# Performance work log

Measured on AMD Instinct MI355X. Metric: run time of the kernel, lower is better.

The kernel has to match this reference:

```python
import jax, jax.numpy as jnp
import numpy as np

QUANT_RANGE = 2688.0  # 6 (max E2M1) * 448 (max E4M3), tllm static_6 rule
EPS = 1e-12
BLOCK = 16  # NVFP4 block size along K


def _round_e2m1(v):
    # Round to the E2M1 grid {0, .5, 1, 1.5, 2, 3, 4, 6} (signed), RTNE on the grid.
    a = jnp.abs(v)
    # quantization step doubles with the exponent: 0.5 for |a|<2, 1 for [2,4), 2 for [4,6]
    e = jnp.floor(jnp.log2(jnp.maximum(a, 1e-30)))
    step = jnp.exp2(jnp.maximum(e, 0.0) - 1.0)
    q = jnp.minimum(jnp.round(a / step) * step, 6.0)
    return jnp.sign(v) * q


def _round_e4m3(v):
    # FP8 E4M3 round-trip (block scale factors are stored as E4M3)
    return v.astype(jnp.float8_e4m3fn).astype(jnp.float32)


def _fp4_quantize(t2d, global_scale):
    # t2d: [R, K] -> (e2m1 codes [R, K/16, 16], e4m3 block scales [R, K/16])
    R, K = t2d.shape
    tb = t2d.reshape(R, K // BLOCK, BLOCK)
    block_amax = jnp.max(jnp.abs(tb), axis=-1)            # [R, K/16]
    sf = _round_e4m3(block_amax * global_scale / 6.0)      # FP8 scale per block
    sf_safe = jnp.maximum(sf, EPS)
    q = _round_e2m1(tb * (global_scale / sf_safe)[..., None])
    return q, sf


def _nvfp4_linear(x, weight, bias):
    in_features = weight.shape[1]
    out_features = weight.shape[0]
    orig_shape = x.shape
    x2 = x.reshape(-1, in_features)                        # [M, K]
    M = x2.shape[0]

    # weight quantization (done once at from_linear time in the original)
    w_amax = jnp.maximum(jnp.max(jnp.abs(weight)), EPS)
    w_gs = QUANT_RANGE / w_amax
    qw, sfw = _fp4_quantize(weight, w_gs)                  # [N, K/16, 16], [N, K/16]

    # dynamic activation quantization
    a_amax = jnp.maximum(jnp.max(jnp.abs(x2)), EPS)
    a_gs = QUANT_RANGE / a_amax
    qx, sfx = _fp4_quantize(x2, a_gs)                      # [M, K/16, 16], [M, K/16]

    # alpha = act_amax * (weight_amax / quant_range^2)
    alpha = a_amax * w_amax / (QUANT_RANGE * QUANT_RANGE)

    # block-scaled GEMM: out[m,n] = alpha * sum_b sfx[m,b] sfw[n,b] (qx[m,b,:] . qw[n,b,:])
    # fused as a dense GEMM over per-block-scaled codes (mathematically identical)
    dx = (qx * sfx[..., None]).reshape(M, in_features)
    dw = (qw * sfw[..., None]).reshape(out_features, in_features)
    out = alpha * (dx @ dw.T) + bias
    return out.reshape(*orig_shape[:-1], out_features)


def setup_inputs() -> dict:
    key = jax.random.key(0)
    k1, k2, k3 = jax.random.split(key, 3)
    x = jax.random.normal(k1, (2, 2048, 4096), dtype=jnp.float32)
    weight = jax.random.normal(k2, (4096, 4096), dtype=jnp.float32) * 0.02
    bias = jax.random.normal(k3, (4096,), dtype=jnp.float32) * 0.01
    return {"x": x, "weight": weight, "bias": bias}


def reference(x, weight, bias):
    return _nvfp4_linear(x, weight, bias)
```

## Files before the change

### kernel.cpp

```cpp
#include <hip/hip_runtime.h>
#include <hip/hip_bf16.h>


typedef unsigned short u16;
typedef __bf16 bf16x8 __attribute__((ext_vector_type(8)));
typedef float f32x4 __attribute__((ext_vector_type(4)));
typedef unsigned short u16x8 __attribute__((ext_vector_type(8)));

#define GLD_LDS(gsrc, ldst)                                                     \
  __builtin_amdgcn_global_load_lds(                                             \
      (const __attribute__((address_space(1))) void*)(gsrc),                    \
      (__attribute__((address_space(3))) void*)(ldst), 16, 0, 0)

#define SBAR()                                                                  \
  do {                                                                          \
    asm volatile("" ::: "memory");                                              \
    __builtin_amdgcn_s_barrier();                                               \
    asm volatile("" ::: "memory");                                              \
  } while (0)

#define KEEP4(S) asm volatile("" ::"v"(S[0]), "v"(S[1]), "v"(S[2]), "v"(S[3]))


__device__ __forceinline__ float round_e4m3(float v) {
  if (v < 0.015625f) {
    return rintf(v * 512.0f) * 0.001953125f;
  }
  unsigned b = __float_as_uint(v);
  unsigned e = (b >> 23) & 0xFFu;
  float step = __uint_as_float((e - 3u) << 23);
  return rintf(v / step) * step;
}

__device__ __forceinline__ float round_e2m1(float v) {
  float a = fabsf(v);
  float step = (a < 2.0f) ? 0.5f : ((a < 4.0f) ? 1.0f : 2.0f);
  float q = fminf(rintf(a / step) * step, 6.0f);
  return copysignf(q, v);
}


__global__ void nvfp4_amax_kernel(const float* __restrict__ x,
                                  const float* __restrict__ w,
                                  unsigned* __restrict__ sc, int nx4, int nw4) {
  const float4* src = blockIdx.y ? (const float4*)w : (const float4*)x;
  int n4 = blockIdx.y ? nw4 : nx4;
  float m = 0.f;
  for (int i = blockIdx.x * blockDim.x + threadIdx.x; i < n4;
       i += gridDim.x * blockDim.x) {
    float4 v = src[i];
    m = fmaxf(m, fmaxf(fmaxf(fabsf(v.x), fabsf(v.y)),
                       fmaxf(fabsf(v.z), fabsf(v.w))));
  }
#pragma unroll
  for (int off = 32; off; off >>= 1) m = fmaxf(m, __shfl_down(m, off));
  __shared__ float red[4];
  if ((threadIdx.x & 63) == 0) red[threadIdx.x >> 6] = m;
  __syncthreads();
  if (threadIdx.x == 0) {
    m = fmaxf(fmaxf(red[0], red[1]), fmaxf(red[2], red[3]));
    atomicMax(&sc[blockIdx.y], __float_as_uint(m));
  }
}


__global__ void nvfp4_quant_kernel(const float* __restrict__ x,
                                   const float* __restrict__ w,
                                   u16* __restrict__ dx, u16* __restrict__ dw,
                                   const unsigned* __restrict__ sc,
                                   int nx4, int nw4) {
  int g = blockIdx.x * blockDim.x + threadIdx.x;
  const float* src; u16* dst; int which, i4;
  if (g < nx4) { src = x; dst = dx; which = 0; i4 = g; }
  else {
    i4 = g - nx4; if (i4 >= nw4) return;
    src = w; dst = dw; which = 1;
  }
  float4 v = ((const float4*)src)[i4];

  float m = fmaxf(fmaxf(fabsf(v.x), fabsf(v.y)), fmaxf(fabsf(v.z), fabsf(v.w)));
  m = fmaxf(m, __shfl_xor(m, 1));
  m = fmaxf(m, __shfl_xor(m, 2));

  float amax = fmaxf(__uint_as_float(sc[which]), 1e-12f);
  float gs = 2688.0f / amax;
  float sf = round_e4m3((m * gs) / 6.0f);
  float sfs = fmaxf(sf, 1e-12f);
  float r = gs / sfs;

  ushort4 o;
  o.x = (u16)(__float_as_uint(round_e2m1(v.x * r) * sf) >> 16);
  o.y = (u16)(__float_as_uint(round_e2m1(v.y * r) * sf) >> 16);
  o.z = (u16)(__float_as_uint(round_e2m1(v.z * r) * sf) >> 16);
  o.w = (u16)(__float_as_uint(round_e2m1(v.w * r) * sf) >> 16);
  ((ushort4*)dst)[i4] = o;
}


#define BM 256
#define BN 256
#define BK 32

__global__ __launch_bounds__(512, 2) void nvfp4_gemm_kernel(
    const u16* __restrict__ A,
    const u16* __restrict__ B,
    const float* __restrict__ bias, const unsigned* __restrict__ sc,
    float* __restrict__ C, int M, int N, int K) {
  __shared__ u16 lA[4][BM * BK];
  __shared__ u16 lB[4][BN * BK];

  const int tid = threadIdx.x;
  const int lane = tid & 63;
  const int wv = tid >> 6;
  const int wm = wv >> 2;
  const int wn = wv & 3;

  const int bid = blockIdx.x;
  const int xcd = bid & 7, loc = bid >> 3;
  const int tm0 = ((xcd & 3) * 4 + (loc & 3)) * BM;
  const int tn0 = ((xcd >> 2) * 8 + (loc >> 2)) * BN;

  const int srow = tid >> 2;
  const int skey = (srow >> 1) & 3;
  const int scol = ((tid & 3) ^ skey) * 8;
  const u16* gA0 = A + (size_t)(tm0 + srow) * K + scol;
  const u16* gA1 = A + (size_t)(tm0 + 128 + srow) * K + scol;
  const u16* gB0 = B + (size_t)(tn0 + srow) * K + scol;
  const u16* gB1 = B + (size_t)(tn0 + 128 + srow) * K + scol;
  const int ld0 = tid * 8;
  const int ld1 = tid * 8 + 4096;

#define STAGE_A(tt)                                                             \
  do {                                                                          \
    int _b = (tt) & 3;                                                          \
    GLD_LDS(gA0 + (size_t)(tt) * BK, &lA[_b][ld0]);                             \
    GLD_LDS(gA1 + (size_t)(tt) * BK, &lA[_b][ld1]);                             \
  } while (0)
#define STAGE_B(tt)                                                             \
  do {                                                                          \
    int _b = (tt) & 3;                                                          \
    GLD_LDS(gB0 + (size_t)(tt) * BK, &lB[_b][ld0]);                             \
    GLD_LDS(gB1 + (size_t)(tt) * BK, &lB[_b][ld1]);                             \
  } while (0)

  const int rb = lane & 15;
  const int cc = (((lane >> 4) ^ ((rb >> 1) & 3)) << 3);
  const int arow = wm * 128 + rb;
  const int brow = wn * 64 + rb;

  f32x4 acc[8][4] = {};
  const int NT = K / BK;
  const int NG = NT / 2;

  STAGE_A(0); STAGE_B(0);
  STAGE_A(1); STAGE_B(1);
  STAGE_A(2); STAGE_B(2);
  asm volatile("s_waitcnt vmcnt(8)" ::: "memory");
  SBAR();

  bf16x8 av[4], aw[4], bve[4], bvo[4];

  for (int g = 0; g < NG; ++g) {
    const int t0 = 2 * g, t1 = 2 * g + 1;
    const int s0 = 2 * g + 3, s1 = 2 * g + 4;
    const u16* bufA0 = lA[t0 & 3];
    const u16* bufB0 = lB[t0 & 3];
    const u16* bufA1 = lA[t1 & 3];
    const u16* bufB1 = lB[t1 & 3];

#pragma unroll
    for (int j = 0; j < 4; ++j)
      bve[j] = *(const bf16x8*)(bufB0 + (brow + j * 16) * BK + cc);
#pragma unroll
    for (int i = 0; i < 4; ++i)
      av[i] = *(const bf16x8*)(bufA0 + (arow + i * 16) * BK + cc);
    if (s0 < NT) STAGE_A(s0);
    SBAR();
    __builtin_amdgcn_s_setprio(1);
#pragma unroll
    for (int i = 0; i < 4; ++i)
#pragma unroll
      for (int j = 0; j < 4; ++j)
        acc[i][j] = __builtin_amdgcn_mfma_f32_16x16x32_bf16(av[i], bve[j],
                                                            acc[i][j], 0, 0, 0);
    __builtin_amdgcn_s_setprio(0);
    SBAR();

#pragma unroll
    for (int i = 0; i < 4; ++i)
      aw[i] = *(const bf16x8*)(bufA0 + (arow + 64 + i * 16) * BK + cc);
    if (s0 < NT) STAGE_B(s0);
    SBAR();
    __builtin_amdgcn_s_setprio(1);
#pragma unroll
    for (int i = 0; i < 4; ++i)
#pragma unroll
      for (int j = 0; j < 4; ++j)
        acc[4 + i][j] = __builtin_amdgcn_mfma_f32_16x16x32_bf16(aw[i], bve[j],
                                                                acc[4 + i][j],
                                                                0, 0, 0);
    __builtin_amdgcn_s_setprio(0);
    KEEP4(av);
    if (g < NG - 1) asm volatile("s_waitcnt vmcnt(8)" ::: "memory");
    else            asm volatile("s_waitcnt vmcnt(0)" ::: "memory");
    SBAR();

#pragma unroll
    for (int j = 0; j < 4; ++j)
      bvo[j] = *(const bf16x8*)(bufB1 + (brow + j * 16) * BK + cc);
#pragma unroll
    for (int i = 0; i < 4; ++i)
      av[i] = *(const bf16x8*)(bufA1 + (arow + i * 16) * BK + cc);
    if (s1 < NT) STAGE_A(s1);
    SBAR();
    __builtin_amdgcn_s_setprio(1);
#pragma unroll
    for (int i = 0; i < 4; ++i)
#pragma unroll
      for (int j = 0; j < 4; ++j)
        acc[i][j] = __builtin_amdgcn_mfma_f32_16x16x32_bf16(av[i], bvo[j],
                                                            acc[i][j], 0, 0, 0);
    __builtin_amdgcn_s_setprio(0);
    SBAR();

#pragma unroll
    for (int i = 0; i < 4; ++i)
      aw[i] = *(const bf16x8*)(bufA1 + (arow + 64 + i * 16) * BK + cc);
    if (s1 < NT) STAGE_B(s1);
    SBAR();
    __builtin_amdgcn_s_setprio(1);
#pragma unroll
    for (int i = 0; i < 4; ++i)
#pragma unroll
      for (int j = 0; j < 4; ++j)
        acc[4 + i][j] = __builtin_amdgcn_mfma_f32_16x16x32_bf16(aw[i], bvo[j],
                                                                acc[4 + i][j],
                                                                0, 0, 0);
    __builtin_amdgcn_s_setprio(0);
    KEEP4(bve);
    KEEP4(av);
    KEEP4(aw);
    if (g < NG - 2)       asm volatile("s_waitcnt vmcnt(8)" ::: "memory");
    else if (g == NG - 2) asm volatile("s_waitcnt vmcnt(4)" ::: "memory");
    SBAR();
  }

  float ax = fmaxf(__uint_as_float(sc[0]), 1e-12f);
  float aw_ = fmaxf(__uint_as_float(sc[1]), 1e-12f);
  float alpha = (ax * aw_) / 7225344.0f;

  const int orow = (lane >> 4) * 4;
  const int ocol = lane & 15;
#pragma unroll
  for (int ai = 0; ai < 8; ++ai) {
#pragma unroll
    for (int j = 0; j < 4; ++j) {
      int col = tn0 + wn * 64 + j * 16 + ocol;
      float bvv = bias[col];
#pragma unroll
      for (int rr = 0; rr < 4; ++rr) {
        int row = tm0 + wm * 128 + ai * 16 + orow + rr;
        C[(size_t)row * N + col] = alpha * acc[ai][j][rr] + bvv;
      }
    }
  }
#undef STAGE_A
#undef STAGE_B
}


extern "C" void kernel_launch(void* const* d_in, const int* in_sizes, int n_in,
                              void* d_out, int out_size, void* d_ws, size_t ws_size,
                              hipStream_t stream) {
  const float* x = (const float*)d_in[0];
  const float* w = (const float*)d_in[1];
  const float* bias = (const float*)d_in[2];
  float* out = (float*)d_out;

  const int N = in_sizes[2];
  const int K = in_sizes[1] / N;
  const int M = in_sizes[0] / K;

  unsigned char* ws = (unsigned char*)d_ws;
  unsigned* sc = (unsigned*)ws;
  u16* dx = (u16*)(ws + 256);
  u16* dw = (u16*)(ws + 256 + (size_t)M * K * sizeof(u16));

  hipMemsetAsync(sc, 0, 8, stream);

  const int nx4 = M * K / 4, nw4 = N * K / 4;
  nvfp4_amax_kernel<<<dim3(1024, 2), 256, 0, stream>>>(x, w, sc, nx4, nw4);

  nvfp4_quant_kernel<<<(nx4 + nw4 + 255) / 256, 256, 0, stream>>>(
      x, w, dx, dw, sc, nx4, nw4);

  nvfp4_gemm_kernel<<<dim3((M / BM) * (N / BN)), 512, 0, stream>>>(
      dx, dw, bias, sc, out, M, N, K);
}
```

Before: 197.0 us.

## Shrink GEMM tile to 256x128 with 4 waves and triple-buffered LDS

The bf16 GEMM moves from a 256x256 tile with 8 waves and a 4-stage LDS ring to a 256x128 tile with 4 waves and a 3-stage ring. Block-to-tile mapping, staging addresses and waitcnt counts are rebuilt to match. The aim is to double the block count for better CU fill and to cut LDS per block so more blocks fit per CU. The cost is less operand reuse per block, more global traffic for A, and a shallower prefetch pipeline.

```diff
diff --git a/kernel.cpp b/kernel.cpp
--- a/kernel.cpp
+++ b/kernel.cpp
@@ -5,7 +5,6 @@
 typedef unsigned short u16;
 typedef __bf16 bf16x8 __attribute__((ext_vector_type(8)));
 typedef float f32x4 __attribute__((ext_vector_type(4)));
-typedef unsigned short u16x8 __attribute__((ext_vector_type(8)));
 
 #define GLD_LDS(gsrc, ldst)                                                     \
   __builtin_amdgcn_global_load_lds(                                             \
@@ -18,8 +17,6 @@
     __builtin_amdgcn_s_barrier();                                               \
     asm volatile("" ::: "memory");                                              \
   } while (0)
-
-#define KEEP4(S) asm volatile("" ::"v"(S[0]), "v"(S[1]), "v"(S[2]), "v"(S[3]))
 
 
 __device__ __forceinline__ float round_e4m3(float v) {
@@ -98,151 +95,149 @@
 
 
 #define BM 256
-#define BN 256
+#define BN 128
 #define BK 32
 
-__global__ __launch_bounds__(512, 2) void nvfp4_gemm_kernel(
+__global__ __launch_bounds__(256, 2) void nvfp4_gemm_kernel(
     const u16* __restrict__ A,
     const u16* __restrict__ B,
     const float* __restrict__ bias, const unsigned* __restrict__ sc,
     float* __restrict__ C, int M, int N, int K) {
-  __shared__ u16 lA[4][BM * BK];
-  __shared__ u16 lB[4][BN * BK];
+  __shared__ u16 lA[3][BM * BK];
+  __shared__ u16 lB[3][BN * BK];
 
   const int tid = threadIdx.x;
   const int lane = tid & 63;
   const int wv = tid >> 6;
-  const int wm = wv >> 2;
-  const int wn = wv & 3;
+  const int wm = wv >> 1;
+  const int wn = wv & 1;
 
   const int bid = blockIdx.x;
   const int xcd = bid & 7, loc = bid >> 3;
-  const int tm0 = ((xcd & 3) * 4 + (loc & 3)) * BM;
-  const int tn0 = ((xcd >> 2) * 8 + (loc >> 2)) * BN;
-
-  const int srow = tid >> 2;
-  const int skey = (srow >> 1) & 3;
-  const int scol = ((tid & 3) ^ skey) * 8;
-  const u16* gA0 = A + (size_t)(tm0 + srow) * K + scol;
-  const u16* gA1 = A + (size_t)(tm0 + 128 + srow) * K + scol;
-  const u16* gB0 = B + (size_t)(tn0 + srow) * K + scol;
-  const u16* gB1 = B + (size_t)(tn0 + 128 + srow) * K + scol;
-  const int ld0 = tid * 8;
-  const int ld1 = tid * 8 + 4096;
-
-#define STAGE_A(tt)                                                             \
+  const int tm0 = (xcd * 2 + (loc >> 5)) * BM;
+  const int tn0 = (loc & 31) * BN;
+
+  const int r4 = lane >> 2;
+  const int swz = ((lane & 3) ^ ((lane >> 3) & 3)) * 8;
+  const u16* gAa[4]; const u16* gBb[2];
+#pragma unroll
+  for (int i = 0; i < 4; ++i)
+    gAa[i] = A + (size_t)(tm0 + (i * 4 + wv) * 16 + r4) * K + swz;
+#pragma unroll
+  for (int i = 0; i < 2; ++i)
+    gBb[i] = B + (size_t)(tn0 + (i * 4 + wv) * 16 + r4) * K + swz;
+  const int ldw = wv * 512 + lane * 8;
+
+#define STAGE_A(tt, bf)                                                         \
   do {                                                                          \
-    int _b = (tt) & 3;                                                          \
-    GLD_LDS(gA0 + (size_t)(tt) * BK, &lA[_b][ld0]);                             \
-    GLD_LDS(gA1 + (size_t)(tt) * BK, &lA[_b][ld1]);                             \
+    _Pragma("unroll") for (int _i = 0; _i < 4; ++_i)                            \
+        GLD_LDS(gAa[_i] + (size_t)(tt) * BK, &lA[bf][_i * 2048 + ldw]);         \
   } while (0)
-#define STAGE_B(tt)                                                             \
+#define STAGE_B(tt, bf)                                                         \
   do {                                                                          \
-    int _b = (tt) & 3;                                                          \
-    GLD_LDS(gB0 + (size_t)(tt) * BK, &lB[_b][ld0]);                             \
-    GLD_LDS(gB1 + (size_t)(tt) * BK, &lB[_b][ld1]);                             \
+    _Pragma("unroll") for (int _i = 0; _i < 2; ++_i)                            \
+        GLD_LDS(gBb[_i] + (size_t)(tt) * BK, &lB[bf][_i * 2048 + ldw]);         \
   } while (0)
 
   const int rb = lane & 15;
   const int cc = (((lane >> 4) ^ ((rb >> 1) & 3)) << 3);
-  const int arow = wm * 128 + rb;
-  const int brow = wn * 64 + rb;
+  const int aoff = (wm * 128 + rb) * BK + cc;
+  const int boff = (wn * 64 + rb) * BK + cc;
 
   f32x4 acc[8][4] = {};
   const int NT = K / BK;
   const int NG = NT / 2;
 
-  STAGE_A(0); STAGE_B(0);
-  STAGE_A(1); STAGE_B(1);
-  STAGE_A(2); STAGE_B(2);
-  asm volatile("s_waitcnt vmcnt(8)" ::: "memory");
+  STAGE_A(0, 0); STAGE_B(0, 0);
+  STAGE_A(1, 1); STAGE_B(1, 1);
+  asm volatile("s_waitcnt vmcnt(6)" ::: "memory");
   SBAR();
 
-  bf16x8 av[4], aw[4], bve[4], bvo[4];
+  bf16x8 av[4], aw[4], bv[4];
+  int cur = 0;
 
   for (int g = 0; g < NG; ++g) {
-    const int t0 = 2 * g, t1 = 2 * g + 1;
-    const int s0 = 2 * g + 3, s1 = 2 * g + 4;
-    const u16* bufA0 = lA[t0 & 3];
-    const u16* bufB0 = lB[t0 & 3];
-    const u16* bufA1 = lA[t1 & 3];
-    const u16* bufB1 = lB[t1 & 3];
+    int t1b = cur + 1; if (t1b == 3) t1b = 0;
+    int s0b = t1b + 1; if (s0b == 3) s0b = 0;
+    const int s0 = 2 * g + 2, s1 = 2 * g + 3;
+    const u16* bufA0 = lA[cur];
+    const u16* bufB0 = lB[cur];
+    const u16* bufA1 = lA[t1b];
+    const u16* bufB1 = lB[t1b];
+    const bool st = (g < NG - 1);
 
 #pragma unroll
     for (int j = 0; j < 4; ++j)
-      bve[j] = *(const bf16x8*)(bufB0 + (brow + j * 16) * BK + cc);
-#pragma unroll
-    for (int i = 0; i < 4; ++i)
-      av[i] = *(const bf16x8*)(bufA0 + (arow + i * 16) * BK + cc);
-    if (s0 < NT) STAGE_A(s0);
-    SBAR();
-    __builtin_amdgcn_s_setprio(1);
-#pragma unroll
-    for (int i = 0; i < 4; ++i)
-#pragma unroll
-      for (int j = 0; j < 4; ++j)
-        acc[i][j] = __builtin_amdgcn_mfma_f32_16x16x32_bf16(av[i], bve[j],
+      bv[j] = *(const bf16x8*)(bufB0 + boff + j * 512);
+#pragma unroll
+    for (int i = 0; i < 4; ++i)
+      av[i] = *(const bf16x8*)(bufA0 + aoff + i * 512);
+    if (st) STAGE_A(s0, s0b);
+    SBAR();
+    __builtin_amdgcn_s_setprio(1);
+#pragma unroll
+    for (int i = 0; i < 4; ++i)
+#pragma unroll
+      for (int j = 0; j < 4; ++j)
+        acc[i][j] = __builtin_amdgcn_mfma_f32_16x16x32_bf16(av[i], bv[j],
                                                             acc[i][j], 0, 0, 0);
     __builtin_amdgcn_s_setprio(0);
     SBAR();
 
 #pragma unroll
     for (int i = 0; i < 4; ++i)
-      aw[i] = *(const bf16x8*)(bufA0 + (arow + 64 + i * 16) * BK + cc);
-    if (s0 < NT) STAGE_B(s0);
-    SBAR();
-    __builtin_amdgcn_s_setprio(1);
-#pragma unroll
-    for (int i = 0; i < 4; ++i)
-#pragma unroll
-      for (int j = 0; j < 4; ++j)
-        acc[4 + i][j] = __builtin_amdgcn_mfma_f32_16x16x32_bf16(aw[i], bve[j],
+      aw[i] = *(const bf16x8*)(bufA0 + aoff + 2048 + i * 512);
+    if (st) STAGE_B(s0, s0b);
+    SBAR();
+    __builtin_amdgcn_s_setprio(1);
+#pragma unroll
+    for (int i = 0; i < 4; ++i)
+#pragma unroll
+      for (int j = 0; j < 4; ++j)
+        acc[4 + i][j] = __builtin_amdgcn_mfma_f32_16x16x32_bf16(aw[i], bv[j],
                                                                 acc[4 + i][j],
                                                                 0, 0, 0);
     __builtin_amdgcn_s_setprio(0);
-    KEEP4(av);
-    if (g < NG - 1) asm volatile("s_waitcnt vmcnt(8)" ::: "memory");
-    else            asm volatile("s_waitcnt vmcnt(0)" ::: "memory");
+    if (st) asm volatile("s_waitcnt vmcnt(6)" ::: "memory");
+    else    asm volatile("s_waitcnt vmcnt(0)" ::: "memory");
     SBAR();
 
 #pragma unroll
     for (int j = 0; j < 4; ++j)
-      bvo[j] = *(const bf16x8*)(bufB1 + (brow + j * 16) * BK + cc);
-#pragma unroll
-    for (int i = 0; i < 4; ++i)
-      av[i] = *(const bf16x8*)(bufA1 + (arow + i * 16) * BK + cc);
-    if (s1 < NT) STAGE_A(s1);
-    SBAR();
-    __builtin_amdgcn_s_setprio(1);
-#pragma unroll
-    for (int i = 0; i < 4; ++i)
-#pragma unroll
-      for (int j = 0; j < 4; ++j)
-        acc[i][j] = __builtin_amdgcn_mfma_f32_16x16x32_bf16(av[i], bvo[j],
+      bv[j] = *(const bf16x8*)(bufB1 + boff + j * 512);
+#pragma unroll
+    for (int i = 0; i < 4; ++i)
+      av[i] = *(const bf16x8*)(bufA1 + aoff + i * 512);
+    if (st) STAGE_A(s1, cur);
+    SBAR();
+    __builtin_amdgcn_s_setprio(1);
+#pragma unroll
+    for (int i = 0; i < 4; ++i)
+#pragma unroll
+      for (int j = 0; j < 4; ++j)
+        acc[i][j] = __builtin_amdgcn_mfma_f32_16x16x32_bf16(av[i], bv[j],
                                                             acc[i][j], 0, 0, 0);
     __builtin_amdgcn_s_setprio(0);
     SBAR();
 
 #pragma unroll
     for (int i = 0; i < 4; ++i)
-      aw[i] = *(const bf16x8*)(bufA1 + (arow + 64 + i * 16) * BK + cc);
-    if (s1 < NT) STAGE_B(s1);
-    SBAR();
-    __builtin_amdgcn_s_setprio(1);
-#pragma unroll
-    for (int i = 0; i < 4; ++i)
-#pragma unroll
-      for (int j = 0; j < 4; ++j)
-        acc[4 + i][j] = __builtin_amdgcn_mfma_f32_16x16x32_bf16(aw[i], bvo[j],
+      aw[i] = *(const bf16x8*)(bufA1 + aoff + 2048 + i * 512);
+    if (st) STAGE_B(s1, cur);
+    SBAR();
+    __builtin_amdgcn_s_setprio(1);
+#pragma unroll
+    for (int i = 0; i < 4; ++i)
+#pragma unroll
+      for (int j = 0; j < 4; ++j)
+        acc[4 + i][j] = __builtin_amdgcn_mfma_f32_16x16x32_bf16(aw[i], bv[j],
                                                                 acc[4 + i][j],
                                                                 0, 0, 0);
     __builtin_amdgcn_s_setprio(0);
-    KEEP4(bve);
-    KEEP4(av);
-    KEEP4(aw);
-    if (g < NG - 2)       asm volatile("s_waitcnt vmcnt(8)" ::: "memory");
-    else if (g == NG - 2) asm volatile("s_waitcnt vmcnt(4)" ::: "memory");
-    SBAR();
+    if (st) asm volatile("s_waitcnt vmcnt(6)" ::: "memory");
+    SBAR();
+
+    cur = s0b;
   }
 
   float ax = fmaxf(__uint_as_float(sc[0]), 1e-12f);
@@ -294,6 +289,6 @@
   nvfp4_quant_kernel<<<(nx4 + nw4 + 255) / 256, 256, 0, stream>>>(
       x, w, dx, dw, sc, nx4, nw4);
 
-  nvfp4_gemm_kernel<<<dim3((M / BM) * (N / BN)), 512, 0, stream>>>(
+  nvfp4_gemm_kernel<<<dim3((M / BM) * (N / BN)), 256, 0, stream>>>(
       dx, dw, bias, sc, out, M, N, K);
 }
```

Measured after the change: 207.1 us. +5.2%, slower.

## Switch GEMM inner loop from 16x16x32 to 32x32x16 bf16 MFMA tiles

Applied to the files above, without the earlier changes.

Replaces the 16x16x32 MFMA tiling with 32x32x16 MFMA instructions. The LDS fragment reads, the LDS XOR swizzle key and the accumulator/epilogue row mapping all change to match. Larger MFMA tiles give more math per fragment read and fewer LDS reads per FLOP. In exchange the epilogue scatters 16 rows per lane with a different store pattern, and the correctness of the new swizzle depends on matching the LDS write and read keys.

```diff
diff --git a/kernel.cpp b/kernel.cpp
--- a/kernel.cpp
+++ b/kernel.cpp
@@ -4,8 +4,7 @@
 
 typedef unsigned short u16;
 typedef __bf16 bf16x8 __attribute__((ext_vector_type(8)));
-typedef float f32x4 __attribute__((ext_vector_type(4)));
-typedef unsigned short u16x8 __attribute__((ext_vector_type(8)));
+typedef float f32x16 __attribute__((ext_vector_type(16)));
 
 #define GLD_LDS(gsrc, ldst)                                                     \
   __builtin_amdgcn_global_load_lds(                                             \
@@ -121,8 +120,7 @@
   const int tn0 = ((xcd >> 2) * 8 + (loc >> 2)) * BN;
 
   const int srow = tid >> 2;
-  const int skey = (srow >> 1) & 3;
-  const int scol = ((tid & 3) ^ skey) * 8;
+  const int scol = ((tid & 3) ^ (srow & 3)) * 8;
   const u16* gA0 = A + (size_t)(tm0 + srow) * K + scol;
   const u16* gA1 = A + (size_t)(tm0 + 128 + srow) * K + scol;
   const u16* gB0 = B + (size_t)(tn0 + srow) * K + scol;
@@ -143,12 +141,15 @@
     GLD_LDS(gB1 + (size_t)(tt) * BK, &lB[_b][ld1]);                             \
   } while (0)
 
-  const int rb = lane & 15;
-  const int cc = (((lane >> 4) ^ ((rb >> 1) & 3)) << 3);
-  const int arow = wm * 128 + rb;
-  const int brow = wn * 64 + rb;
-
-  f32x4 acc[8][4] = {};
+  const int l31 = lane & 31;
+  const int kq = lane >> 5;
+  const int key = lane & 3;
+  const int cc0 = ((0 * 2 + kq) ^ key) * 8;
+  const int cc1 = ((1 * 2 + kq) ^ key) * 8;
+  const int arow = wm * 128 + l31;
+  const int brow = wn * 64 + l31;
+
+  f32x16 acc[4][2] = {};
   const int NT = K / BK;
   const int NG = NT / 2;
 
@@ -159,6 +160,33 @@
   SBAR();
 
   bf16x8 av[4], aw[4], bve[4], bvo[4];
+
+#define READ_AF(DST, buf, mtbase)                                               \
+  do {                                                                          \
+    DST[0] = *(const bf16x8*)((buf) + (arow + (mtbase) * 32) * BK + cc0);       \
+    DST[1] = *(const bf16x8*)((buf) + (arow + (mtbase) * 32) * BK + cc1);       \
+    DST[2] = *(const bf16x8*)((buf) + (arow + (mtbase) * 32 + 32) * BK + cc0);  \
+    DST[3] = *(const bf16x8*)((buf) + (arow + (mtbase) * 32 + 32) * BK + cc1);  \
+  } while (0)
+#define READ_BF(DST, buf)                                                       \
+  do {                                                                          \
+    DST[0] = *(const bf16x8*)((buf) + (brow) * BK + cc0);                       \
+    DST[1] = *(const bf16x8*)((buf) + (brow) * BK + cc1);                       \
+    DST[2] = *(const bf16x8*)((buf) + (brow + 32) * BK + cc0);                  \
+    DST[3] = *(const bf16x8*)((buf) + (brow + 32) * BK + cc1);                  \
+  } while (0)
+
+#define MFMA8(AF, BF, a0)                                                       \
+  do {                                                                          \
+    acc[a0][0]     = __builtin_amdgcn_mfma_f32_32x32x16_bf16(AF[0], BF[0], acc[a0][0], 0, 0, 0);     \
+    acc[a0][1]     = __builtin_amdgcn_mfma_f32_32x32x16_bf16(AF[0], BF[2], acc[a0][1], 0, 0, 0);     \
+    acc[a0 + 1][0] = __builtin_amdgcn_mfma_f32_32x32x16_bf16(AF[2], BF[0], acc[a0 + 1][0], 0, 0, 0); \
+    acc[a0 + 1][1] = __builtin_amdgcn_mfma_f32_32x32x16_bf16(AF[2], BF[2], acc[a0 + 1][1], 0, 0, 0); \
+    acc[a0][0]     = __builtin_amdgcn_mfma_f32_32x32x16_bf16(AF[1], BF[1], acc[a0][0], 0, 0, 0);     \
+    acc[a0][1]     = __builtin_amdgcn_mfma_f32_32x32x16_bf16(AF[1], BF[3], acc[a0][1], 0, 0, 0);     \
+    acc[a0 + 1][0] = __builtin_amdgcn_mfma_f32_32x32x16_bf16(AF[3], BF[1], acc[a0 + 1][0], 0, 0, 0); \
+    acc[a0 + 1][1] = __builtin_amdgcn_mfma_f32_32x32x16_bf16(AF[3], BF[3], acc[a0 + 1][1], 0, 0, 0); \
+  } while (0)
 
   for (int g = 0; g < NG; ++g) {
     const int t0 = 2 * g, t1 = 2 * g + 1;
@@ -168,74 +196,40 @@
     const u16* bufA1 = lA[t1 & 3];
     const u16* bufB1 = lB[t1 & 3];
 
-#pragma unroll
-    for (int j = 0; j < 4; ++j)
-      bve[j] = *(const bf16x8*)(bufB0 + (brow + j * 16) * BK + cc);
-#pragma unroll
-    for (int i = 0; i < 4; ++i)
-      av[i] = *(const bf16x8*)(bufA0 + (arow + i * 16) * BK + cc);
+    READ_BF(bve, bufB0);
+    READ_AF(av, bufA0, 0);
     if (s0 < NT) STAGE_A(s0);
     SBAR();
     __builtin_amdgcn_s_setprio(1);
-#pragma unroll
-    for (int i = 0; i < 4; ++i)
-#pragma unroll
-      for (int j = 0; j < 4; ++j)
-        acc[i][j] = __builtin_amdgcn_mfma_f32_16x16x32_bf16(av[i], bve[j],
-                                                            acc[i][j], 0, 0, 0);
-    __builtin_amdgcn_s_setprio(0);
-    SBAR();
-
-#pragma unroll
-    for (int i = 0; i < 4; ++i)
-      aw[i] = *(const bf16x8*)(bufA0 + (arow + 64 + i * 16) * BK + cc);
+    MFMA8(av, bve, 0);
+    __builtin_amdgcn_s_setprio(0);
+    SBAR();
+
+    READ_AF(aw, bufA0, 2);
     if (s0 < NT) STAGE_B(s0);
     SBAR();
     __builtin_amdgcn_s_setprio(1);
-#pragma unroll
-    for (int i = 0; i < 4; ++i)
-#pragma unroll
-      for (int j = 0; j < 4; ++j)
-        acc[4 + i][j] = __builtin_amdgcn_mfma_f32_16x16x32_bf16(aw[i], bve[j],
-                                                                acc[4 + i][j],
-                                                                0, 0, 0);
+    MFMA8(aw, bve, 2);
     __builtin_amdgcn_s_setprio(0);
     KEEP4(av);
     if (g < NG - 1) asm volatile("s_waitcnt vmcnt(8)" ::: "memory");
     else            asm volatile("s_waitcnt vmcnt(0)" ::: "memory");
     SBAR();
 
-#pragma unroll
-    for (int j = 0; j < 4; ++j)
-      bvo[j] = *(const bf16x8*)(bufB1 + (brow + j * 16) * BK + cc);
-#pragma unroll
-    for (int i = 0; i < 4; ++i)
-      av[i] = *(const bf16x8*)(bufA1 + (arow + i * 16) * BK + cc);
+    READ_BF(bvo, bufB1);
+    READ_AF(av, bufA1, 0);
     if (s1 < NT) STAGE_A(s1);
     SBAR();
     __builtin_amdgcn_s_setprio(1);
-#pragma unroll
-    for (int i = 0; i < 4; ++i)
-#pragma unroll
-      for (int j = 0; j < 4; ++j)
-        acc[i][j] = __builtin_amdgcn_mfma_f32_16x16x32_bf16(av[i], bvo[j],
-                                                            acc[i][j], 0, 0, 0);
-    __builtin_amdgcn_s_setprio(0);
-    SBAR();
-
-#pragma unroll
-    for (int i = 0; i < 4; ++i)
-      aw[i] = *(const bf16x8*)(bufA1 + (arow + 64 + i * 16) * BK + cc);
+    MFMA8(av, bvo, 0);
+    __builtin_amdgcn_s_setprio(0);
+    SBAR();
+
+    READ_AF(aw, bufA1, 2);
     if (s1 < NT) STAGE_B(s1);
     SBAR();
     __builtin_amdgcn_s_setprio(1);
-#pragma unroll
-    for (int i = 0; i < 4; ++i)
-#pragma unroll
-      for (int j = 0; j < 4; ++j)
-        acc[4 + i][j] = __builtin_amdgcn_mfma_f32_16x16x32_bf16(aw[i], bvo[j],
-                                                                acc[4 + i][j],
-                                                                0, 0, 0);
+    MFMA8(aw, bvo, 2);
     __builtin_amdgcn_s_setprio(0);
     KEEP4(bve);
     KEEP4(av);
@@ -249,23 +243,24 @@
   float aw_ = fmaxf(__uint_as_float(sc[1]), 1e-12f);
   float alpha = (ax * aw_) / 7225344.0f;
 
-  const int orow = (lane >> 4) * 4;
-  const int ocol = lane & 15;
-#pragma unroll
-  for (int ai = 0; ai < 8; ++ai) {
-#pragma unroll
-    for (int j = 0; j < 4; ++j) {
-      int col = tn0 + wn * 64 + j * 16 + ocol;
+#pragma unroll
+  for (int mt = 0; mt < 4; ++mt) {
+#pragma unroll
+    for (int nt = 0; nt < 2; ++nt) {
+      int col = tn0 + wn * 64 + nt * 32 + l31;
       float bvv = bias[col];
 #pragma unroll
-      for (int rr = 0; rr < 4; ++rr) {
-        int row = tm0 + wm * 128 + ai * 16 + orow + rr;
-        C[(size_t)row * N + col] = alpha * acc[ai][j][rr] + bvv;
+      for (int reg = 0; reg < 16; ++reg) {
+        int row = tm0 + wm * 128 + mt * 32 + (reg & 3) + 8 * (reg >> 2) + 4 * kq;
+        C[(size_t)row * N + col] = alpha * acc[mt][nt][reg] + bvv;
       }
     }
   }
 #undef STAGE_A
 #undef STAGE_B
+#undef READ_AF
+#undef READ_BF
+#undef MFMA8
 }
 
 
```

Result: slower. 226.8 us (+15.1%).
